# Kernel tuning notes

Hardware: AMD Instinct MI355X
Metric: run time of the kernel (lower is better)

Reference implementation:

```python
import jax, jax.numpy as jnp
import numpy as np

D_MODEL = 1024
N_HEADS = 16
D_Q = 64
D_V = 64
N_SEG = 16
EPS_LN = 1e-5
EPS_MEM = 1e-6


def setup_inputs() -> dict:
    key = jax.random.key(0)
    ks = jax.random.split(key, 10)
    N, T = 4, 4096
    inp = {
        "query_sequences": jax.random.normal(ks[0], (N, T, D_MODEL), dtype=jnp.float32),
        "key_sequences": jax.random.normal(ks[1], (N, T, D_MODEL), dtype=jnp.float32),
        "value_sequences": jax.random.normal(ks[2], (N, T, D_MODEL), dtype=jnp.float32),
        "Wq": jax.random.normal(ks[3], (D_MODEL, N_HEADS * D_Q), dtype=jnp.float32) * 0.02,
        "Wk": jax.random.normal(ks[4], (D_MODEL, N_HEADS * D_Q), dtype=jnp.float32) * 0.02,
        "Wv": jax.random.normal(ks[5], (D_MODEL, N_HEADS * D_V), dtype=jnp.float32) * 0.02,
        "Wo": jax.random.normal(ks[6], (N_HEADS * D_V, D_MODEL), dtype=jnp.float32) * 0.02,
        "ln_w": jnp.ones((D_MODEL,), dtype=jnp.float32),
        "ln_b": jnp.zeros((D_MODEL,), dtype=jnp.float32),
        "beta": jnp.ones((1,), dtype=jnp.float32),
    }
    return inp


def _layer_norm(x, w, b):
    mu = jnp.mean(x, axis=-1, keepdims=True)
    var = jnp.var(x, axis=-1, keepdims=True)
    return (x - mu) * jax.lax.rsqrt(var + EPS_LN) * w + b


def reference(query_sequences, key_sequences, value_sequences, Wq, Wk, Wv, Wo, ln_w, ln_b, beta):
    N, t, _ = query_sequences.shape
    S = t // N_SEG  # segment length (256)

    # qkv_norm applied to q, and (self-attention) to k and v as well
    qn = _layer_norm(query_sequences, ln_w, ln_b)
    kn = _layer_norm(key_sequences, ln_w, ln_b)
    vn = _layer_norm(value_sequences, ln_w, ln_b)

    # project and split heads -> [N, H, t, d]
    qh = (qn @ Wq).reshape(N, t, N_HEADS, D_Q).transpose(0, 2, 1, 3)
    kh = (kn @ Wk).reshape(N, t, N_HEADS, D_Q).transpose(0, 2, 1, 3)
    vh = (vn @ Wv).reshape(N, t, N_HEADS, D_V).transpose(0, 2, 1, 3)

    # segment: [N_SEG, N, H, S, d] so lax.scan iterates segments sequentially
    seg = lambda x, d: x.reshape(N, N_HEADS, N_SEG, S, d).transpose(2, 0, 1, 3, 4)
    q_segs, k_segs, v_segs = seg(qh, D_Q), seg(kh, D_Q), seg(vh, D_V)

    b_gate = jax.nn.sigmoid(beta)[0]            # scalar mixing gate
    scale = 1.0 / np.sqrt(D_Q).astype(np.float32)
    causal = jnp.tril(jnp.ones((S, S), dtype=bool))

    def step(carry, xs):
        mem, z = carry                          # [N,H,Dq,Dv], [N,H,Dq]
        qs, ks_, vs = xs                        # [N,H,S,d]
        sq = jax.nn.elu(qs) + 1.0
        sk = jax.nn.elu(ks_) + 1.0
        # retrieve from compressive memory
        num = jnp.einsum('nhsd,nhde->nhse', sq, mem)
        den = jnp.einsum('nhsd,nhd->nhs', sq, z)[..., None] + EPS_MEM
        a_mem = num / den                       # [N,H,S,Dv]
        # local causal softmax attention within the segment
        scores = jnp.einsum('nhsd,nhtd->nhst', qs, ks_) * scale
        scores = jnp.where(causal, scores, -jnp.inf)
        probs = jax.nn.softmax(scores, axis=-1)
        attn = jnp.einsum('nhst,nhtd->nhsd', probs, vs)
        out = b_gate * a_mem + (1.0 - b_gate) * attn
        # linear memory update
        mem = mem + jnp.einsum('nhsd,nhse->nhde', sk, vs)
        z = z + sk.sum(axis=2)
        return (mem, z), out

    mem0 = jnp.zeros((N, N_HEADS, D_Q, D_V), dtype=query_sequences.dtype)
    z0 = jnp.zeros((N, N_HEADS, D_Q), dtype=query_sequences.dtype)
    _, outs = jax.lax.scan(step, (mem0, z0), (q_segs, k_segs, v_segs))

    # outs: [N_SEG, N, H, S, Dv] -> [N, t, H*Dv]
    seqs = outs.transpose(1, 0, 3, 2, 4).reshape(N, t, N_HEADS * D_V)
    return seqs @ Wo
```

## Files before the change

### kernel.cpp

```cpp
#include <hip/hip_runtime.h>
#include <stdint.h>
#include <math.h>


typedef __attribute__((ext_vector_type(8))) short bf16x8_t;
typedef __attribute__((ext_vector_type(4))) short short4_t;
typedef __attribute__((ext_vector_type(4))) float f32x4;

__device__ __forceinline__ float bf2f(short s){
  union { unsigned u; float f; } v; v.u = ((unsigned)(unsigned short)s) << 16; return v.f;
}
__device__ __forceinline__ short f2bf(float f){
  union { float fl; unsigned u; } v; v.fl = f;
  unsigned r = v.u + 0x7FFFu + ((v.u >> 16) & 1u);
  return (short)(unsigned short)(r >> 16);
}
__device__ __forceinline__ f32x4 mfma16(bf16x8_t a, bf16x8_t b, f32x4 c){
  return __builtin_amdgcn_mfma_f32_16x16x32_bf16(a, b, c, 0, 0, 0);
}
__device__ __forceinline__ void gl_lds16(const short* g, short* l){
  __builtin_amdgcn_global_load_lds((const __attribute__((address_space(1))) void*)g,
                                   (__attribute__((address_space(3))) void*)l, 16, 0, 0);
}

__global__ __launch_bounds__(256) void ln3(const float* __restrict__ xq, const float* __restrict__ xk,
                                           const float* __restrict__ xv,
                                           const float* __restrict__ gw, const float* __restrict__ gb,
                                           short* __restrict__ oq, short* __restrict__ ok,
                                           short* __restrict__ ov){
  const int row = blockIdx.x, which = blockIdx.y, tid = threadIdx.x;
  const float* x = which == 0 ? xq : which == 1 ? xk : xv;
  short* out     = which == 0 ? oq : which == 1 ? ok : ov;
  const float4 v = *reinterpret_cast<const float4*>(x + (size_t)row*1024 + tid*4);
  float s  = v.x + v.y + v.z + v.w;
  float s2 = v.x*v.x + v.y*v.y + v.z*v.z + v.w*v.w;
  #pragma unroll
  for (int off = 1; off < 64; off <<= 1){
    s  += __shfl_xor(s,  off);
    s2 += __shfl_xor(s2, off);
  }
  __shared__ float red[8];
  if ((tid & 63) == 0){ red[tid>>6] = s; red[4 + (tid>>6)] = s2; }
  __syncthreads();
  s  = red[0] + red[1] + red[2] + red[3];
  s2 = red[4] + red[5] + red[6] + red[7];
  const float mu  = s * (1.0f/1024.0f);
  const float var = s2 * (1.0f/1024.0f) - mu*mu;
  const float rs  = rsqrtf(var + 1e-5f);
  const float4 wv = *reinterpret_cast<const float4*>(gw + tid*4);
  const float4 bv = *reinterpret_cast<const float4*>(gb + tid*4);
  short4_t o;
  o[0] = f2bf((v.x-mu)*rs*wv.x + bv.x);
  o[1] = f2bf((v.y-mu)*rs*wv.y + bv.y);
  o[2] = f2bf((v.z-mu)*rs*wv.z + bv.z);
  o[3] = f2bf((v.w-mu)*rs*wv.w + bv.w);
  *reinterpret_cast<short4_t*>(out + (size_t)row*1024 + tid*4) = o;
}

__global__ __launch_bounds__(256) void wcast4(const float* __restrict__ W0, const float* __restrict__ W1,
                                              const float* __restrict__ W2, const float* __restrict__ W3,
                                              short* __restrict__ T0, short* __restrict__ T1,
                                              short* __restrict__ T2, short* __restrict__ T3){
  const int z = blockIdx.z;
  const float* W = z == 0 ? W0 : z == 1 ? W1 : z == 2 ? W2 : W3;
  short* Wt      = z == 0 ? T0 : z == 1 ? T1 : z == 2 ? T2 : T3;
  __shared__ float tile[64][65];
  const int bx = blockIdx.x, by = blockIdx.y, tid = threadIdx.x;
  #pragma unroll
  for (int p=0;p<4;++p){
    int idx = p*256 + tid;
    int r = idx >> 4, c4 = (idx & 15) << 2;
    const float4 v = *reinterpret_cast<const float4*>(W + (size_t)(by*64 + r)*1024 + bx*64 + c4);
    tile[r][c4+0] = v.x; tile[r][c4+1] = v.y; tile[r][c4+2] = v.z; tile[r][c4+3] = v.w;
  }
  __syncthreads();
  #pragma unroll
  for (int p=0;p<4;++p){
    int idx = p*256 + tid;
    int r = idx >> 4, c4 = (idx & 15) << 2;
    short4_t o;
    o[0] = f2bf(tile[c4+0][r]); o[1] = f2bf(tile[c4+1][r]);
    o[2] = f2bf(tile[c4+2][r]); o[3] = f2bf(tile[c4+3][r]);
    *reinterpret_cast<short4_t*>(Wt + (size_t)(bx*64 + r)*1024 + by*64 + c4) = o;
  }
}

__device__ __forceinline__ void gemm_body(short* smem, const short* __restrict__ A,
                                          const short* __restrict__ Bt, void* __restrict__ C, int mode){
  short* As = smem;
  short* Bs = smem + 32768;
  const int tid = threadIdx.x;
  const int m0 = blockIdx.x * 256;
  const int c0 = blockIdx.y * 256;
  const int lane = tid & 63, wid = tid >> 6;
  const int wr = wid >> 2, wc = wid & 3;
  const int l15 = lane & 15, lhi = lane >> 4;

  const short* Asrc[4]; const short* Bsrc[4];
  #pragma unroll
  for (int p=0;p<4;++p){
    int i = tid + 512*p;
    int r = i >> 3, g = (i & 7) ^ (r & 7);
    Asrc[p] = A  + (size_t)(m0 + r)*1024 + g*8;
    Bsrc[p] = Bt + (size_t)(c0 + r)*1024 + g*8;
  }

  f32x4 acc[8][4];
  #pragma unroll
  for (int m=0;m<8;++m)
    #pragma unroll
    for (int n=0;n<4;++n) acc[m][n] = (f32x4){0.f,0.f,0.f,0.f};

  #define STAGE_A(t) { short* _d=&As[((t)&1)<<14]; int _k=(t)<<6; \
      gl_lds16(Asrc[0]+_k, _d+tid*8); gl_lds16(Asrc[1]+_k, _d+4096+tid*8); \
      gl_lds16(Asrc[2]+_k, _d+8192+tid*8); gl_lds16(Asrc[3]+_k, _d+12288+tid*8); }
  #define STAGE_B(t) { short* _d=&Bs[((t)&1)<<14]; int _k=(t)<<6; \
      gl_lds16(Bsrc[0]+_k, _d+tid*8); gl_lds16(Bsrc[1]+_k, _d+4096+tid*8); \
      gl_lds16(Bsrc[2]+_k, _d+8192+tid*8); gl_lds16(Bsrc[3]+_k, _d+12288+tid*8); }

  STAGE_A(0); STAGE_B(0);
  asm volatile("s_waitcnt vmcnt(0)" ::: "memory");
  __builtin_amdgcn_s_barrier();

  for (int t = 0; t < 16; ++t){
    const short* Ab = &As[(t & 1) << 14];
    const short* Bb = &Bs[(t & 1) << 14];
    if (t < 15){ STAGE_A(t+1); STAGE_B(t+1); }
    bf16x8_t af[4][2], bfr[4][2];
    #pragma unroll
    for (int m=0;m<4;++m){
      int r = wr*128 + m*16 + l15;
      #pragma unroll
      for (int ks=0;ks<2;++ks){
        int sl = (ks*4 + lhi) ^ (r & 7);
        af[m][ks] = *reinterpret_cast<const bf16x8_t*>(&Ab[r*64 + sl*8]);
      }
    }
    #pragma unroll
    for (int n=0;n<2;++n){
      int r = wc*64 + n*16 + l15;
      #pragma unroll
      for (int ks=0;ks<2;++ks){
        int sl = (ks*4 + lhi) ^ (r & 7);
        bfr[n][ks] = *reinterpret_cast<const bf16x8_t*>(&Bb[r*64 + sl*8]);
      }
    }
    __builtin_amdgcn_s_setprio(1);
    #pragma unroll
    for (int m=0;m<4;++m)
      #pragma unroll
      for (int n=0;n<2;++n)
        #pragma unroll
        for (int ks=0;ks<2;++ks)
          acc[m][n] = mfma16(af[m][ks], bfr[n][ks], acc[m][n]);
    __builtin_amdgcn_s_setprio(0);
    #pragma unroll
    for (int n=2;n<4;++n){
      int r = wc*64 + n*16 + l15;
      #pragma unroll
      for (int ks=0;ks<2;++ks){
        int sl = (ks*4 + lhi) ^ (r & 7);
        bfr[n][ks] = *reinterpret_cast<const bf16x8_t*>(&Bb[r*64 + sl*8]);
      }
    }
    __builtin_amdgcn_s_setprio(1);
    #pragma unroll
    for (int m=0;m<4;++m)
      #pragma unroll
      for (int n=2;n<4;++n)
        #pragma unroll
        for (int ks=0;ks<2;++ks)
          acc[m][n] = mfma16(af[m][ks], bfr[n][ks], acc[m][n]);
    __builtin_amdgcn_s_setprio(0);
    #pragma unroll
    for (int m=0;m<4;++m){
      int r = wr*128 + 64 + m*16 + l15;
      #pragma unroll
      for (int ks=0;ks<2;++ks){
        int sl = (ks*4 + lhi) ^ (r & 7);
        af[m][ks] = *reinterpret_cast<const bf16x8_t*>(&Ab[r*64 + sl*8]);
      }
    }
    __builtin_amdgcn_s_setprio(1);
    #pragma unroll
    for (int m=0;m<4;++m)
      #pragma unroll
      for (int n=0;n<2;++n)
        #pragma unroll
        for (int ks=0;ks<2;++ks)
          acc[4+m][n] = mfma16(af[m][ks], bfr[n][ks], acc[4+m][n]);
    __builtin_amdgcn_s_setprio(0);
    __builtin_amdgcn_s_setprio(1);
    #pragma unroll
    for (int m=0;m<4;++m)
      #pragma unroll
      for (int n=2;n<4;++n)
        #pragma unroll
        for (int ks=0;ks<2;++ks)
          acc[4+m][n] = mfma16(af[m][ks], bfr[n][ks], acc[4+m][n]);
    __builtin_amdgcn_s_setprio(0);
    asm volatile("s_waitcnt vmcnt(0)" ::: "memory");
    __builtin_amdgcn_s_barrier();
  }
  #undef STAGE_A
  #undef STAGE_B

  if (mode == 0){
    short* Cb = (short*)C;
    #pragma unroll
    for (int m=0;m<8;++m)
      #pragma unroll
      for (int n=0;n<4;++n)
        #pragma unroll
        for (int j=0;j<4;++j){
          int row = m0 + wr*128 + m*16 + lhi*4 + j;
          int col = c0 + wc*64 + n*16 + l15;
          size_t oidx = ((size_t)((row>>12)*16 + (col>>6)) * 4096 + (size_t)(row & 4095)) * 64 + (col & 63);
          Cb[oidx] = f2bf(acc[m][n][j]);
        }
  } else if (mode == 2){
    short* Cb = (short*)C;
    #pragma unroll
    for (int m=0;m<8;++m)
      #pragma unroll
      for (int n=0;n<4;++n){
        int rowb = m0 + wr*128 + m*16 + lhi*4;
        int col  = c0 + wc*64 + n*16 + l15;
        int nh = ((rowb>>12)<<4) + (col>>6);
        int e  = col & 63;
        int tt = rowb & 4095;
        short4_t o;
        #pragma unroll
        for (int j=0;j<4;++j) o[j] = f2bf(acc[m][n][j]);
        *reinterpret_cast<short4_t*>(&Cb[((size_t)nh*64 + e)*4096 + tt]) = o;
      }
  } else {
    float* Cf = (float*)C;
    #pragma unroll
    for (int m=0;m<8;++m)
      #pragma unroll
      for (int n=0;n<4;++n)
        #pragma unroll
        for (int j=0;j<4;++j){
          int row = m0 + wr*128 + m*16 + lhi*4 + j;
          int col = c0 + wc*64 + n*16 + l15;
          Cf[(size_t)row*1024 + col] = acc[m][n][j];
        }
  }
}

__global__ __launch_bounds__(512, 2) void gemm_qkv(const short* __restrict__ A0, const short* __restrict__ A1,
    const short* __restrict__ A2, const short* __restrict__ B0, const short* __restrict__ B1,
    const short* __restrict__ B2, short* __restrict__ C0, short* __restrict__ C1, short* __restrict__ C2){
  extern __shared__ short smem[];
  const int z = blockIdx.z;
  const short* A = z == 0 ? A0 : z == 1 ? A1 : A2;
  const short* B = z == 0 ? B0 : z == 1 ? B1 : B2;
  short* C       = z == 0 ? C0 : z == 1 ? C1 : C2;
  gemm_body(smem, A, B, (void*)C, z == 2 ? 2 : 0);
}

__global__ __launch_bounds__(512, 2) void gemm_wo(const short* __restrict__ A, const short* __restrict__ Bt,
                                                  float* __restrict__ C){
  extern __shared__ short smem[];
  gemm_body(smem, A, Bt, (void*)C, 1);
}

__global__ __launch_bounds__(256) void stageA(const short* __restrict__ kh, const short* __restrict__ vhT,
                                              short* __restrict__ delta_b, float* __restrict__ zd){
  const int seg = blockIdx.x, nh = blockIdx.y, tid = threadIdx.x;
  const int lane = tid & 63, w = tid >> 6;
  const int l15 = lane & 15, lhi = lane >> 4;
  __shared__ short skT[64*256];
  const size_t thead = (size_t)nh*4096 + (size_t)seg*256;

  #pragma unroll
  for (int ch=0; ch<8; ++ch){
    int s  = ch*32 + (tid>>3);
    int lc = (tid&7)*8;
    bf16x8_t kv = *reinterpret_cast<const bf16x8_t*>(kh + (thead + s)*64 + lc);
    #pragma unroll
    for (int j=0;j<8;++j){
      float f = bf2f(kv[j]);
      short sv = f2bf((f > 0.f) ? (f + 1.f) : __expf(f));
      int d = lc + j;
      int bo = ((d*256 + s) << 1) ^ (((d>>3)&7) << 4);
      *reinterpret_cast<short*>(reinterpret_cast<char*>(skT) + bo) = sv;
    }
  }
  __syncthreads();

  bf16x8_t ones;
  #pragma unroll
  for (int i=0;i<8;++i) ones[i] = (short)0x3F80;

  f32x4 dacc[4], zacc[4];
  #pragma unroll
  for (int jf=0;jf<4;++jf){ dacc[jf] = (f32x4){0.f,0.f,0.f,0.f}; zacc[jf] = (f32x4){0.f,0.f,0.f,0.f}; }

  #pragma unroll
  for (int ks=0; ks<8; ++ks){
    bf16x8_t av = *reinterpret_cast<const bf16x8_t*>(
        vhT + ((size_t)nh*64 + w*16 + l15)*4096 + (size_t)seg*256 + ks*32 + lhi*8);
    #pragma unroll
    for (int jf=0;jf<4;++jf){
      int d  = jf*16 + l15;
      int so = ks*32 + lhi*8;
      int bo = ((d*256 + so) << 1) ^ (((d>>3)&7) << 4);
      bf16x8_t bk = *reinterpret_cast<const bf16x8_t*>(reinterpret_cast<char*>(skT) + bo);
      dacc[jf] = mfma16(av, bk, dacc[jf]);
      if (w == 0) zacc[jf] = mfma16(ones, bk, zacc[jf]);
    }
  }

  short* dp = delta_b + (size_t)(seg*64 + nh)*4096;
  #pragma unroll
  for (int jf=0;jf<4;++jf)
    #pragma unroll
    for (int j=0;j<4;++j)
      dp[(w*16 + lhi*4 + j)*64 + jf*16 + l15] = f2bf(dacc[jf][j]);
  if (w == 0 && lhi == 0){
    #pragma unroll
    for (int jf=0;jf<4;++jf)
      zd[(size_t)(seg*64 + nh)*64 + jf*16 + l15] = zacc[jf][0];
  }
}

__global__ __launch_bounds__(256) void stageB(const short* __restrict__ delta_b, const float* __restrict__ zd,
                                              short* __restrict__ mpre_b, float* __restrict__ zpre){
  const int c = blockIdx.x, nh = blockIdx.y, tid = threadIdx.x;
  const int idx = c*256 + tid;
  float acc = 0.f;
  for (int seg=0; seg<16; ++seg){
    size_t b = (size_t)(seg*64 + nh)*4096 + idx;
    mpre_b[b] = f2bf(acc);
    acc += bf2f(delta_b[b]);
  }
  if (c == 0 && tid < 64){
    float za = 0.f;
    for (int seg=0; seg<16; ++seg){
      size_t zb = (size_t)(seg*64 + nh)*64 + tid;
      zpre[zb] = za;
      za += zd[zb];
    }
  }
}

__global__ __launch_bounds__(256, 3) void stageC(const short* __restrict__ qh, const short* __restrict__ kh,
    const short* __restrict__ vhT, const short* __restrict__ mpre_b, const float* __restrict__ z_pre,
    const float* __restrict__ beta, short* __restrict__ seqs)
{
  const int seg  = blockIdx.x;
  const int nh   = blockIdx.y;
  const int tid = threadIdx.x;
  const int lane = tid & 63, w = tid >> 6;
  const int l15 = lane & 15, lhi = lane >> 4;

  __shared__ float zl[64];
  __shared__ short pl[4][32][72];

  const size_t thead = (size_t)nh*4096 + (size_t)seg*256;

  if (tid < 64) zl[tid] = z_pre[(size_t)(seg*64 + nh)*64 + tid];
  __syncthreads();

  const float bg = 1.f / (1.f + __expf(-beta[0]));
  const float scale = 0.125f;
  bf16x8_t ones;
  #pragma unroll
  for (int i=0;i<8;++i) ones[i] = (short)0x3F80;
  const short* mpbase = mpre_b + (size_t)(seg*64 + nh)*4096;
  const int nb = nh >> 4, hh = nh & 15;

  for (int p = 0; p < 2; ++p){
    const int tile = p ? (7 - w) : w;
    const int nkt  = (tile >> 1) + 1;
    const int rb   = tile * 32;

    bf16x8_t aq[2][2];
    #pragma unroll
    for (int m=0;m<2;++m)
      #pragma unroll
      for (int ks=0;ks<2;++ks)
        aq[m][ks] = *reinterpret_cast<const bf16x8_t*>(qh + (thead + rb + m*16 + l15)*64 + ks*32 + lhi*8);

    f32x4 o_acc[2][4], l_acc[2];
    #pragma unroll
    for (int m=0;m<2;++m){
      l_acc[m] = (f32x4){0.f,0.f,0.f,0.f};
      #pragma unroll
      for (int jf=0;jf<4;++jf) o_acc[m][jf] = (f32x4){0.f,0.f,0.f,0.f};
    }

    for (int kt = 0; kt < nkt; ++kt){
      bf16x8_t bv[4][2];
      #pragma unroll
      for (int jf=0;jf<4;++jf)
        #pragma unroll
        for (int ks2=0;ks2<2;++ks2)
          bv[jf][ks2] = *reinterpret_cast<const bf16x8_t*>(
              vhT + ((size_t)nh*64 + jf*16 + l15)*4096 + (size_t)seg*256 + kt*64 + ks2*32 + lhi*8);

      f32x4 s_acc[2][4];
      #pragma unroll
      for (int m=0;m<2;++m)
        #pragma unroll
        for (int jf=0;jf<4;++jf) s_acc[m][jf] = (f32x4){0.f,0.f,0.f,0.f};
      #pragma unroll
      for (int ks=0;ks<2;++ks){
        bf16x8_t bk[4];
        #pragma unroll
        for (int jf=0;jf<4;++jf)
          bk[jf] = *reinterpret_cast<const bf16x8_t*>(kh + (thead + kt*64 + jf*16 + l15)*64 + ks*32 + lhi*8);
        #pragma unroll
        for (int m=0;m<2;++m)
          #pragma unroll
          for (int jf=0;jf<4;++jf)
            s_acc[m][jf] = mfma16(aq[m][ks], bk[jf], s_acc[m][jf]);
      }
      const bool lastkt = (kt == nkt - 1);
      #pragma unroll
      for (int m=0;m<2;++m)
        #pragma unroll
        for (int jf=0;jf<4;++jf)
          #pragma unroll
          for (int j=0;j<4;++j){
            float vv = s_acc[m][jf][j] * scale;
            if (lastkt){
              int sr = rb + m*16 + lhi*4 + j;
              int tc = kt*64 + jf*16 + l15;
              if (tc > sr) vv = -INFINITY;
            }
            float pv = __expf(vv);
            pl[w][m*16 + lhi*4 + j][jf*16 + l15] = f2bf(pv);
          }
      #pragma unroll
      for (int ks2=0;ks2<2;++ks2){
        bf16x8_t ap[2];
        #pragma unroll
        for (int m=0;m<2;++m)
          ap[m] = *reinterpret_cast<const bf16x8_t*>(&pl[w][m*16 + l15][ks2*32 + lhi*8]);
        #pragma unroll
        for (int m=0;m<2;++m){
          l_acc[m] = mfma16(ap[m], ones, l_acc[m]);
          #pragma unroll
          for (int jf=0;jf<4;++jf)
            o_acc[m][jf] = mfma16(ap[m], bv[jf][ks2], o_acc[m][jf]);
        }
      }
    }

    bf16x8_t sq[2][2];
    #pragma unroll
    for (int m=0;m<2;++m)
      #pragma unroll
      for (int ks=0;ks<2;++ks)
        #pragma unroll
        for (int i=0;i<8;++i){
          float f = bf2f(aq[m][ks][i]);
          sq[m][ks][i] = f2bf((f > 0.f) ? (f + 1.f) : __expf(f));
        }
    bf16x8_t bz[2];
    #pragma unroll
    for (int ks=0;ks<2;++ks)
      #pragma unroll
      for (int i=0;i<8;++i) bz[ks][i] = f2bf(zl[ks*32 + lhi*8 + i]);

    f32x4 n_acc[2][4], d_acc[2];
    #pragma unroll
    for (int m=0;m<2;++m){
      d_acc[m] = (f32x4){0.f,0.f,0.f,0.f};
      #pragma unroll
      for (int jf=0;jf<4;++jf) n_acc[m][jf] = (f32x4){0.f,0.f,0.f,0.f};
    }
    #pragma unroll
    for (int ks=0;ks<2;++ks){
      bf16x8_t bm[4];
      #pragma unroll
      for (int jf=0;jf<4;++jf)
        bm[jf] = *reinterpret_cast<const bf16x8_t*>(mpbase + (jf*16 + l15)*64 + ks*32 + lhi*8);
      #pragma unroll
      for (int m=0;m<2;++m){
        #pragma unroll
        for (int jf=0;jf<4;++jf) n_acc[m][jf] = mfma16(sq[m][ks], bm[jf], n_acc[m][jf]);
        d_acc[m] = mfma16(sq[m][ks], bz[ks], d_acc[m]);
      }
    }

    #pragma unroll
    for (int m=0;m<2;++m)
      #pragma unroll
      for (int jf=0;jf<4;++jf)
        #pragma unroll
        for (int j=0;j<4;++j){
          float attn = o_acc[m][jf][j] / l_acc[m][j];
          float amem = n_acc[m][jf][j] / (d_acc[m][j] + 1e-6f);
          float ov = bg*amem + (1.f-bg)*attn;
          int srow = rb + m*16 + lhi*4 + j;
          seqs[((size_t)nb*4096 + (size_t)seg*256 + srow)*1024 + hh*64 + jf*16 + l15] = f2bf(ov);
        }
  }
}

extern "C" void kernel_launch(void* const* d_in, const int* in_sizes, int n_in,
                              void* d_out, int out_size, void* d_ws, size_t ws_size,
                              hipStream_t stream){
  (void)in_sizes; (void)n_in; (void)out_size; (void)ws_size;
  const float* q    = (const float*)d_in[0];
  const float* k    = (const float*)d_in[1];
  const float* v    = (const float*)d_in[2];
  const float* Wq   = (const float*)d_in[3];
  const float* Wk   = (const float*)d_in[4];
  const float* Wv   = (const float*)d_in[5];
  const float* Wo   = (const float*)d_in[6];
  const float* lnw  = (const float*)d_in[7];
  const float* lnb  = (const float*)d_in[8];
  const float* beta = (const float*)d_in[9];
  char* ws = (char*)d_ws;
  const size_t MB = 1024ull*1024ull;
  short* WqT    = (short*)(ws + 0*MB);
  short* WkT    = (short*)(ws + 2*MB);
  short* WvT    = (short*)(ws + 4*MB);
  short* WoT    = (short*)(ws + 6*MB);
  short* xn_v   = (short*)(ws + 8*MB);
  short* seqs   = xn_v;
  short* qh     = (short*)(ws + 40*MB);
  short* kh     = (short*)(ws + 72*MB);
  short* vhT    = (short*)(ws + 104*MB);
  short* delta_b= (short*)(ws + 136*MB);
  float* zd     = (float*)(ws + 144*MB);
  short* mpre_b = (short*)(ws + 145*MB);
  float* zpre   = (float*)(ws + 153*MB);
  short* xn_q   = (short*)d_out;
  short* xn_k   = (short*)d_out + 16384ull*1024ull;

  wcast4<<<dim3(16,16,4),256,0,stream>>>(Wq,Wk,Wv,Wo, WqT,WkT,WvT,WoT);
  ln3<<<dim3(16384,3),256,0,stream>>>(q,k,v, lnw,lnb, xn_q,xn_k,xn_v);

  const size_t lds_gemm = 131072;
  gemm_qkv<<<dim3(64,4,3),512,lds_gemm,stream>>>(xn_q,xn_k,xn_v, WqT,WkT,WvT, qh,kh,vhT);

  stageA<<<dim3(16,64),256,0,stream>>>(kh, vhT, delta_b, zd);
  stageB<<<dim3(16,64),256,0,stream>>>(delta_b, zd, mpre_b, zpre);
  stageC<<<dim3(16,64),256,0,stream>>>(qh, kh, vhT, mpre_b, zpre, beta, seqs);
  gemm_wo<<<dim3(64,4),512,lds_gemm,stream>>>(seqs, WoT, (float*)d_out);
}
```

Measured before the change: 315.3 us.

## Switch GEMM to 4-stage K=32 pipeline with triple-prefetch async LDS loads

Result: slower. 326.8 us (+3.6%).

```diff
diff --git a/kernel.cpp b/kernel.cpp
--- a/kernel.cpp
+++ b/kernel.cpp
@@ -96,11 +96,11 @@
   const int wr = wid >> 2, wc = wid & 3;
   const int l15 = lane & 15, lhi = lane >> 4;
 
-  const short* Asrc[4]; const short* Bsrc[4];
-  #pragma unroll
-  for (int p=0;p<4;++p){
+  const short* Asrc[2]; const short* Bsrc[2];
+  #pragma unroll
+  for (int p=0;p<2;++p){
     int i = tid + 512*p;
-    int r = i >> 3, g = (i & 7) ^ (r & 7);
+    int r = i >> 2, g = (i & 3) ^ (r & 3) ^ ((r >> 2) & 3);
     Asrc[p] = A  + (size_t)(m0 + r)*1024 + g*8;
     Bsrc[p] = Bt + (size_t)(c0 + r)*1024 + g*8;
   }
@@ -111,99 +111,44 @@
     #pragma unroll
     for (int n=0;n<4;++n) acc[m][n] = (f32x4){0.f,0.f,0.f,0.f};
 
-  #define STAGE_A(t) { short* _d=&As[((t)&1)<<14]; int _k=(t)<<6; \
-      gl_lds16(Asrc[0]+_k, _d+tid*8); gl_lds16(Asrc[1]+_k, _d+4096+tid*8); \
-      gl_lds16(Asrc[2]+_k, _d+8192+tid*8); gl_lds16(Asrc[3]+_k, _d+12288+tid*8); }
-  #define STAGE_B(t) { short* _d=&Bs[((t)&1)<<14]; int _k=(t)<<6; \
-      gl_lds16(Bsrc[0]+_k, _d+tid*8); gl_lds16(Bsrc[1]+_k, _d+4096+tid*8); \
-      gl_lds16(Bsrc[2]+_k, _d+8192+tid*8); gl_lds16(Bsrc[3]+_k, _d+12288+tid*8); }
-
-  STAGE_A(0); STAGE_B(0);
-  asm volatile("s_waitcnt vmcnt(0)" ::: "memory");
+  #define STAGE(t) { short* _a=&As[((t)&3)<<13]; short* _b=&Bs[((t)&3)<<13]; int _k=(t)<<5; \
+      gl_lds16(Asrc[0]+_k, _a+tid*8); gl_lds16(Asrc[1]+_k, _a+4096+tid*8); \
+      gl_lds16(Bsrc[0]+_k, _b+tid*8); gl_lds16(Bsrc[1]+_k, _b+4096+tid*8); }
+
+  STAGE(0); STAGE(1); STAGE(2);
+  asm volatile("s_waitcnt vmcnt(8)" ::: "memory");
   __builtin_amdgcn_s_barrier();
 
-  for (int t = 0; t < 16; ++t){
-    const short* Ab = &As[(t & 1) << 14];
-    const short* Bb = &Bs[(t & 1) << 14];
-    if (t < 15){ STAGE_A(t+1); STAGE_B(t+1); }
-    bf16x8_t af[4][2], bfr[4][2];
-    #pragma unroll
-    for (int m=0;m<4;++m){
+  for (int t = 0; t < 32; ++t){
+    const short* Ab = &As[(t & 3) << 13];
+    const short* Bb = &Bs[(t & 3) << 13];
+    if (t < 29) STAGE(t+3);
+    bf16x8_t af[8], bfr[4];
+    #pragma unroll
+    for (int m=0;m<8;++m){
       int r = wr*128 + m*16 + l15;
-      #pragma unroll
-      for (int ks=0;ks<2;++ks){
-        int sl = (ks*4 + lhi) ^ (r & 7);
-        af[m][ks] = *reinterpret_cast<const bf16x8_t*>(&Ab[r*64 + sl*8]);
-      }
-    }
-    #pragma unroll
-    for (int n=0;n<2;++n){
+      int sl = lhi ^ (r & 3) ^ ((r >> 2) & 3);
+      af[m] = *reinterpret_cast<const bf16x8_t*>(&Ab[r*32 + sl*8]);
+    }
+    #pragma unroll
+    for (int n=0;n<4;++n){
       int r = wc*64 + n*16 + l15;
-      #pragma unroll
-      for (int ks=0;ks<2;++ks){
-        int sl = (ks*4 + lhi) ^ (r & 7);
-        bfr[n][ks] = *reinterpret_cast<const bf16x8_t*>(&Bb[r*64 + sl*8]);
-      }
+      int sl = lhi ^ (r & 3) ^ ((r >> 2) & 3);
+      bfr[n] = *reinterpret_cast<const bf16x8_t*>(&Bb[r*32 + sl*8]);
     }
     __builtin_amdgcn_s_setprio(1);
     #pragma unroll
-    for (int m=0;m<4;++m)
-      #pragma unroll
-      for (int n=0;n<2;++n)
-        #pragma unroll
-        for (int ks=0;ks<2;++ks)
-          acc[m][n] = mfma16(af[m][ks], bfr[n][ks], acc[m][n]);
+    for (int m=0;m<8;++m)
+      #pragma unroll
+      for (int n=0;n<4;++n)
+        acc[m][n] = mfma16(af[m], bfr[n], acc[m][n]);
     __builtin_amdgcn_s_setprio(0);
-    #pragma unroll
-    for (int n=2;n<4;++n){
-      int r = wc*64 + n*16 + l15;
-      #pragma unroll
-      for (int ks=0;ks<2;++ks){
-        int sl = (ks*4 + lhi) ^ (r & 7);
-        bfr[n][ks] = *reinterpret_cast<const bf16x8_t*>(&Bb[r*64 + sl*8]);
-      }
-    }
-    __builtin_amdgcn_s_setprio(1);
-    #pragma unroll
-    for (int m=0;m<4;++m)
-      #pragma unroll
-      for (int n=2;n<4;++n)
-        #pragma unroll
-        for (int ks=0;ks<2;++ks)
-          acc[m][n] = mfma16(af[m][ks], bfr[n][ks], acc[m][n]);
-    __builtin_amdgcn_s_setprio(0);
-    #pragma unroll
-    for (int m=0;m<4;++m){
-      int r = wr*128 + 64 + m*16 + l15;
-      #pragma unroll
-      for (int ks=0;ks<2;++ks){
-        int sl = (ks*4 + lhi) ^ (r & 7);
-        af[m][ks] = *reinterpret_cast<const bf16x8_t*>(&Ab[r*64 + sl*8]);
-      }
-    }
-    __builtin_amdgcn_s_setprio(1);
-    #pragma unroll
-    for (int m=0;m<4;++m)
-      #pragma unroll
-      for (int n=0;n<2;++n)
-        #pragma unroll
-        for (int ks=0;ks<2;++ks)
-          acc[4+m][n] = mfma16(af[m][ks], bfr[n][ks], acc[4+m][n]);
-    __builtin_amdgcn_s_setprio(0);
-    __builtin_amdgcn_s_setprio(1);
-    #pragma unroll
-    for (int m=0;m<4;++m)
-      #pragma unroll
-      for (int n=2;n<4;++n)
-        #pragma unroll
-        for (int ks=0;ks<2;++ks)
-          acc[4+m][n] = mfma16(af[m][ks], bfr[n][ks], acc[4+m][n]);
-    __builtin_amdgcn_s_setprio(0);
-    asm volatile("s_waitcnt vmcnt(0)" ::: "memory");
-    __builtin_amdgcn_s_barrier();
-  }
-  #undef STAGE_A
-  #undef STAGE_B
+    if (t < 29)       { asm volatile("s_waitcnt vmcnt(8)" ::: "memory"); }
+    else if (t == 29) { asm volatile("s_waitcnt vmcnt(4)" ::: "memory"); }
+    else if (t == 30) { asm volatile("s_waitcnt vmcnt(0)" ::: "memory"); }
+    if (t < 31) __builtin_amdgcn_s_barrier();
+  }
+  #undef STAGE
 
   if (mode == 0){
     short* Cb = (short*)C;
```
